# Kernel tuning notes

Hardware: AMD Instinct MI355X
Metric: run time of the kernel (lower is better)

Reference implementation:

```python
import jax, jax.numpy as jnp
import numpy as np

B, T, IDIM, ODIM, HDIM, CDIM = 8, 8192, 256, 256, 1024, 128


def setup_inputs() -> dict:
    key = jax.random.key(0)
    ks = jax.random.split(key, 7)
    s_enc = 1.0 / np.sqrt(IDIM)
    s_dec = 1.0 / np.sqrt(HDIM)
    return {
        "x": jax.random.normal(ks[0], (B, T, IDIM), jnp.float32),
        "mask_prev": jnp.zeros((B, T, HDIM), jnp.float32),
        "W_enc": jax.random.uniform(ks[1], (IDIM, HDIM), jnp.float32, -s_enc, s_enc),
        "b_enc": jax.random.uniform(ks[2], (HDIM,), jnp.float32, -s_enc, s_enc),
        "W_dec_self": jax.random.uniform(ks[3], (HDIM, IDIM), jnp.float32, -s_dec, s_dec),
        "b_dec_self": jax.random.uniform(ks[4], (IDIM,), jnp.float32, -s_dec, s_dec),
        "W_dec_src": jax.random.uniform(ks[5], (HDIM, ODIM), jnp.float32, -s_dec, s_dec),
        "b_dec_src": jax.random.uniform(ks[6], (ODIM,), jnp.float32, -s_dec, s_dec),
        "decoder_type": 0,  # 0 = 'self', 1 = 'src'
    }


def _topk_masks(h, cdim):
    # energy_pooling_mask with share=True: topk(k=2*cdim) of h^2 along hdim.
    energy = h * h  # [B,T,H]
    _, idx = jax.lax.top_k(energy, 2 * cdim)  # [B,T,2C] indices into H
    bi = jnp.arange(h.shape[0])[:, None, None]
    ti = jnp.arange(h.shape[1])[None, :, None]
    # scatter instead of materializing one_hot [B,T,2C,H]
    mask = jnp.zeros_like(h).at[bi, ti, idx[..., :cdim]].add(1.0)
    mask_share = jnp.zeros_like(h).at[bi, ti, idx].add(1.0)
    return mask, mask_share


def reference(x, mask_prev, W_enc, b_enc, W_dec_self, b_dec_self, W_dec_src, b_dec_src, decoder_type):
    # encoder
    h = jnp.einsum("bti,ih->bth", x, W_enc) + b_enc  # [B,T,H]
    # hidden_exclude_activation (mask_prev provided): zero previously-used units
    h = jnp.where(mask_prev > 0, 0.0, h)
    mask_cur, mask_cur_share = _topk_masks(h, CDIM)
    mask_new = mask_prev + mask_cur
    h = jnp.where(mask_cur_share > 0, h, 0.0)
    # decoder (idim == odim asserted in original)
    if decoder_type == 0:
        out = jnp.einsum("bth,ho->bto", h, W_dec_self) + b_dec_self
    else:
        out = jnp.einsum("bth,ho->bto", h, W_dec_src) + b_dec_src
    return out, mask_new
```

## Files before the change

### kernel.cpp

```cpp
#include <hip/hip_runtime.h>
#include <hip/hip_bf16.h>

#define B_ 8
#define T_ 8192
#define M_ (B_ * T_)
#define IDIM 256
#define HDIM 1024
#define ODIM 256
#define CDIM 128
#define OUT_OFF ((size_t)M_ * ODIM)

typedef __attribute__((ext_vector_type(4))) float floatx4;
typedef __attribute__((ext_vector_type(8))) short shortx8;

__device__ __forceinline__ void glds16(const float* g, void* lds) {
    __builtin_amdgcn_global_load_lds(
        (const __attribute__((address_space(1))) void*)g,
        (__attribute__((address_space(3))) void*)lds, 16, 0, 0);
}

__global__ __launch_bounds__(256) void k0_convw(const float* __restrict__ Wself,
                                                const float* __restrict__ Wsrc,
                                                const int* __restrict__ dtype,
                                                __hip_bfloat16* __restrict__ WdT) {
    int id = blockIdx.x * 256 + threadIdx.x;
    int n = id >> 10;
    int k = id & 1023;
    const float* W = (*dtype == 0) ? Wself : Wsrc;
    WdT[id] = __float2bfloat16(W[(size_t)k * ODIM + n]);
}

__global__ __launch_bounds__(256, 3) void k1_enc(const float* __restrict__ X,
                                                 const float* __restrict__ W,
                                                 const float* __restrict__ bias,
                                                 float* __restrict__ H) {
    __shared__ __align__(16) float As[32][128];
    __shared__ __align__(16) float Bs[2][32][128];
    const int t  = threadIdx.x;
    const int m0 = blockIdx.x * 128;
    const int n0 = blockIdx.y * 128;
    const int tx = t & 15;
    const int ty = t >> 4;
    const int wavebase = t & ~63;

    int acol[4], ak4[4];
    const float* aptr[4];
#pragma unroll
    for (int r = 0; r < 4; ++r) {
        int idx = r * 256 + t;
        int row = idx >> 3;
        int k4  = (idx & 7) << 2;
        ak4[r]  = k4;
        acol[r] = row ^ k4;
        aptr[r] = X + (size_t)(m0 + row) * IDIM + k4;
    }
    const float* bptr[4];
#pragma unroll
    for (int r = 0; r < 4; ++r) {
        int idx = r * 256 + t;
        int row = idx >> 5;
        int c4  = (idx & 31) << 2;
        bptr[r] = W + (size_t)row * HDIM + n0 + c4;
    }

    float acc[8][8];
#pragma unroll
    for (int i = 0; i < 8; ++i)
#pragma unroll
        for (int j = 0; j < 8; ++j) acc[i][j] = 0.0f;

    float4 areg[4];

#pragma unroll
    for (int r = 0; r < 4; ++r) areg[r] = *(const float4*)(aptr[r]);
#pragma unroll
    for (int r = 0; r < 4; ++r)
        glds16(bptr[r], (char*)&Bs[0][0][0] + (size_t)(r * 256 + wavebase) * 16);
#pragma unroll
    for (int r = 0; r < 4; ++r) {
        As[ak4[r] + 0][acol[r]] = areg[r].x;
        As[ak4[r] + 1][acol[r]] = areg[r].y;
        As[ak4[r] + 2][acol[r]] = areg[r].z;
        As[ak4[r] + 3][acol[r]] = areg[r].w;
    }
    asm volatile("s_waitcnt vmcnt(0)");
    __syncthreads();

#pragma unroll 1
    for (int tt = 0; tt < IDIM / 32; ++tt) {
        const int cur = tt & 1;
        if (tt < IDIM / 32 - 1) {
            const int kn = (tt + 1) * 32;
#pragma unroll
            for (int r = 0; r < 4; ++r)
                glds16(bptr[r] + (size_t)kn * HDIM,
                       (char*)&Bs[cur ^ 1][0][0] + (size_t)(r * 256 + wavebase) * 16);
#pragma unroll
            for (int r = 0; r < 4; ++r) areg[r] = *(const float4*)(aptr[r] + kn);
        }

#pragma unroll 8
        for (int k = 0; k < 32; ++k) {
            const int s = k & 28;
            float4 a0 = *(const float4*)&As[k][(ty * 8) ^ s];
            float4 a1 = *(const float4*)&As[k][(ty * 8 + 4) ^ s];
            float4 b0 = *(const float4*)&Bs[cur][k][tx * 4];
            float4 b1 = *(const float4*)&Bs[cur][k][tx * 4 + 64];
#define FMA_ROW(i, ax)                              \
            acc[i][0] = fmaf(ax, b0.x, acc[i][0]);  \
            acc[i][1] = fmaf(ax, b0.y, acc[i][1]);  \
            acc[i][2] = fmaf(ax, b0.z, acc[i][2]);  \
            acc[i][3] = fmaf(ax, b0.w, acc[i][3]);  \
            acc[i][4] = fmaf(ax, b1.x, acc[i][4]);  \
            acc[i][5] = fmaf(ax, b1.y, acc[i][5]);  \
            acc[i][6] = fmaf(ax, b1.z, acc[i][6]);  \
            acc[i][7] = fmaf(ax, b1.w, acc[i][7]);
            FMA_ROW(0, a0.x) FMA_ROW(1, a0.y) FMA_ROW(2, a0.z) FMA_ROW(3, a0.w)
            FMA_ROW(4, a1.x) FMA_ROW(5, a1.y) FMA_ROW(6, a1.z) FMA_ROW(7, a1.w)
#undef FMA_ROW
        }

        if (tt < IDIM / 32 - 1) {
            asm volatile("s_waitcnt vmcnt(0)");
            __syncthreads();
#pragma unroll
            for (int r = 0; r < 4; ++r) {
                As[ak4[r] + 0][acol[r]] = areg[r].x;
                As[ak4[r] + 1][acol[r]] = areg[r].y;
                As[ak4[r] + 2][acol[r]] = areg[r].z;
                As[ak4[r] + 3][acol[r]] = areg[r].w;
            }
            __syncthreads();
        }
    }

#pragma unroll
    for (int i = 0; i < 8; ++i) {
        int gm = m0 + ty * 8 + i;
        float* o = H + (size_t)gm * HDIM + n0;
        float4 v0, v1;
        v0.x = acc[i][0] + bias[n0 + tx * 4 + 0];
        v0.y = acc[i][1] + bias[n0 + tx * 4 + 1];
        v0.z = acc[i][2] + bias[n0 + tx * 4 + 2];
        v0.w = acc[i][3] + bias[n0 + tx * 4 + 3];
        v1.x = acc[i][4] + bias[n0 + 64 + tx * 4 + 0];
        v1.y = acc[i][5] + bias[n0 + 64 + tx * 4 + 1];
        v1.z = acc[i][6] + bias[n0 + 64 + tx * 4 + 2];
        v1.w = acc[i][7] + bias[n0 + 64 + tx * 4 + 3];
        *(float4*)(o + tx * 4) = v0;
        *(float4*)(o + 64 + tx * 4) = v1;
    }
}

#define NBIN 512
#define KBASE 1600
#define CAP 128

__device__ __forceinline__ unsigned int bsearch_kth(const unsigned int* u, int k,
                                                    int lane, int* r_out) {
    unsigned long long lo = 0, hi = 0xFFFFFFFFull;
    while (lo < hi) {
        unsigned int mid = (unsigned int)((lo + hi + 1) >> 1);
        int c = 0;
#pragma unroll
        for (int i = 0; i < 16; ++i) c += (u[i] >= mid) ? 1 : 0;
#pragma unroll
        for (int off = 1; off < 64; off <<= 1) {
            int o = __shfl_down(c, off, 64);
            if (lane + off < 64) c += o;
        }
        c = __shfl(c, 0);
        if (c >= k) lo = mid; else hi = (unsigned long long)mid - 1;
    }
    unsigned int T = (unsigned int)lo;
    int g = 0;
#pragma unroll
    for (int i = 0; i < 16; ++i) g += (u[i] > T) ? 1 : 0;
#pragma unroll
    for (int off = 1; off < 64; off <<= 1) {
        int o = __shfl_down(g, off, 64);
        if (lane + off < 64) g += o;
    }
    g = __shfl(g, 0);
    *r_out = k - g;
    return T;
}

__global__ __launch_bounds__(64) void k2_topk(const float* __restrict__ mask_prev,
                                              float* __restrict__ Hio,
                                              __hip_bfloat16* __restrict__ Abf) {
    __shared__ unsigned int hist[NBIN];
    __shared__ unsigned long long cand[2][CAP];
    __shared__ unsigned int sres[8];
    __shared__ unsigned int scnt[2];
    const int lane = threadIdx.x;
    const size_t row = (size_t)blockIdx.x;
    const float* mp = mask_prev + row * HDIM + lane * 16;
    float* hrow = Hio + row * HDIM + lane * 16;

    float hv[16], mpv[16];
    unsigned int u[16];
    int bin[16];
#pragma unroll
    for (int c = 0; c < 4; ++c) {
        float4 m4 = *(const float4*)(mp + c * 4);
        float4 h4 = *(const float4*)(hrow + c * 4);
        float mm[4] = {m4.x, m4.y, m4.z, m4.w};
        float hh[4] = {h4.x, h4.y, h4.z, h4.w};
#pragma unroll
        for (int x = 0; x < 4; ++x) {
            int i = c * 4 + x;
            float h = (mm[x] > 0.0f) ? 0.0f : hh[x];
            mpv[i] = mm[x]; hv[i] = h;
            u[i] = __float_as_uint(h * h);
            int b = (int)(u[i] >> 19) - KBASE;
            bin[i] = (b < 0) ? 0 : ((b > NBIN - 1) ? NBIN - 1 : b);
        }
    }

#pragma unroll
    for (int q = 0; q < 8; ++q) hist[lane + (q << 6)] = 0u;
    if (lane < 2) scnt[lane] = 0u;
    __syncthreads();
#pragma unroll
    for (int i = 0; i < 16; ++i) atomicAdd(&hist[bin[i]], 1u);
    __syncthreads();

    {
        unsigned int cj[8]; unsigned int lt = 0;
#pragma unroll
        for (int jj = 0; jj < 8; ++jj) { cj[jj] = hist[lane * 8 + jj]; lt += cj[jj]; }
        unsigned int s = lt;
#pragma unroll
        for (int off = 1; off < 64; off <<= 1) {
            unsigned int o = (unsigned int)__shfl_down((int)s, off, 64);
            if (lane + off < 64) s += o;
        }
        unsigned int run = s - lt;
#pragma unroll
        for (int jj = 7; jj >= 0; --jj) {
            unsigned int gt = run, ge = run + cj[jj];
            if (gt < CDIM && CDIM <= ge)         { sres[0] = lane * 8 + jj; sres[1] = CDIM - gt; }
            if (gt < 2 * CDIM && 2 * CDIM <= ge) { sres[2] = lane * 8 + jj; sres[3] = 2 * CDIM - gt; }
            run = ge;
        }
    }
    __syncthreads();
    const unsigned int b1 = sres[0], kk1 = sres[1];
    const unsigned int b2 = sres[2], kk2 = sres[3];

#pragma unroll
    for (int i = 0; i < 16; ++i) {
        int j = lane * 16 + i;
        unsigned long long pk = ((unsigned long long)u[i] << 32) | (unsigned int)(1023 - j);
        if ((unsigned int)bin[i] == b1) {
            unsigned int p = atomicAdd(&scnt[0], 1u);
            if (p < CAP) cand[0][p] = pk;
        }
        if (b2 != b1 && (unsigned int)bin[i] == b2) {
            unsigned int p = atomicAdd(&scnt[1], 1u);
            if (p < CAP) cand[1][p] = pk;
        }
    }
    __syncthreads();
    const unsigned int C1 = scnt[0];
    const unsigned int C2 = (b2 == b1) ? C1 : scnt[1];
    const unsigned long long* L2 = (b2 == b1) ? cand[0] : cand[1];

    if (C1 <= CAP) {
        for (unsigned int idx = lane; idx < C1; idx += 64) {
            unsigned long long mine = cand[0][idx];
            unsigned int myu = (unsigned int)(mine >> 32);
            unsigned int rank = 0, gtu = 0;
            for (unsigned int c = 0; c < C1; ++c) {
                unsigned long long o = cand[0][c];
                rank += (o > mine) ? 1u : 0u;
                gtu  += ((unsigned int)(o >> 32) > myu) ? 1u : 0u;
            }
            if (rank == kk1 - 1) { sres[4] = myu; sres[5] = gtu; }
        }
    }
    if (C2 <= CAP) {
        for (unsigned int idx = lane; idx < C2; idx += 64) {
            unsigned long long mine = L2[idx];
            unsigned int myu = (unsigned int)(mine >> 32);
            unsigned int rank = 0, gtu = 0;
            for (unsigned int c = 0; c < C2; ++c) {
                unsigned long long o = L2[c];
                rank += (o > mine) ? 1u : 0u;
                gtu  += ((unsigned int)(o >> 32) > myu) ? 1u : 0u;
            }
            if (rank == kk2 - 1) { sres[6] = myu; sres[7] = gtu; }
        }
    }
    __syncthreads();

    unsigned int T1, T2; int r1, r2;
    if (C1 <= CAP) { T1 = sres[4]; r1 = (int)(kk1 - sres[5]); }
    else           { T1 = bsearch_kth(u, CDIM, lane, &r1); }
    if (C2 <= CAP) { T2 = sres[6]; r2 = (int)(kk2 - sres[7]); }
    else           { T2 = bsearch_kth(u, 2 * CDIM, lane, &r2); }

    int p1[16], p2[16];
    int tot1 = 0, tot2 = 0;
#pragma unroll
    for (int i = 0; i < 16; ++i) {
        p1[i] = tot1; p2[i] = tot2;
        tot1 += (u[i] == T1) ? 1 : 0;
        tot2 += (u[i] == T2) ? 1 : 0;
    }
    int s1v = tot1, s2v = tot2;
#pragma unroll
    for (int off = 1; off < 64; off <<= 1) {
        int o1 = __shfl_up(s1v, off, 64);
        int o2 = __shfl_up(s2v, off, 64);
        if (lane >= off) { s1v += o1; s2v += o2; }
    }
    const int ex1 = s1v - tot1;
    const int ex2 = s2v - tot2;

#pragma unroll
    for (int c = 0; c < 4; ++c) {
        float v[4];
#pragma unroll
        for (int x = 0; x < 4; ++x) {
            int i = c * 4 + x;
            bool s1 = (u[i] > T1) || ((u[i] == T1) && (ex1 + p1[i] < r1));
            v[x] = mpv[i] + (s1 ? 1.0f : 0.0f);
        }
        float4 v4 = {v[0], v[1], v[2], v[3]};
        *(float4*)(hrow + c * 4) = v4;
    }
    __hip_bfloat16* ab = Abf + row * HDIM + lane * 16;
#pragma unroll
    for (int half = 0; half < 2; ++half) {
        union { unsigned short us[8]; uint4 v; } pk;
#pragma unroll
        for (int x = 0; x < 8; ++x) {
            int i = half * 8 + x;
            bool s2 = (u[i] > T2) || ((u[i] == T2) && (ex2 + p2[i] < r2));
            __hip_bfloat16 bb = __float2bfloat16(s2 ? hv[i] : 0.0f);
            pk.us[x] = *(unsigned short*)&bb;
        }
        *(uint4*)(ab + half * 8) = pk.v;
    }
}

#define K3LD 40
__global__ __launch_bounds__(256) void k3_dec(const __hip_bfloat16* __restrict__ A,
                                              const __hip_bfloat16* __restrict__ Bt,
                                              const float* __restrict__ bias_self,
                                              const float* __restrict__ bias_src,
                                              const int* __restrict__ dtype,
                                              float* __restrict__ Out) {
    __shared__ __align__(16) __hip_bfloat16 As[128 * K3LD];
    __shared__ __align__(16) __hip_bfloat16 Bs[128 * K3LD];
    const int t = threadIdx.x;
    const int lane = t & 63;
    const int wave = t >> 6;
    const int m0 = blockIdx.x * 128;
    const int n0 = blockIdx.y * 128;
    const int wr = wave >> 1;
    const int wc = wave & 1;
    const int quad = lane >> 4;
    const int rf = lane & 15;

    int srow[2], skc[2];
#pragma unroll
    for (int p = 0; p < 2; ++p) {
        int l = p * 256 + t;
        srow[p] = l >> 2;
        skc[p]  = (l & 3) << 3;
    }

    floatx4 acc[4][4];
    const floatx4 z = {0.0f, 0.0f, 0.0f, 0.0f};
#pragma unroll
    for (int i = 0; i < 4; ++i)
#pragma unroll
        for (int j = 0; j < 4; ++j) acc[i][j] = z;

    uint4 apre[2], bpre[2];
#pragma unroll
    for (int p = 0; p < 2; ++p) {
        apre[p] = *(const uint4*)(A  + (size_t)(m0 + srow[p]) * HDIM + skc[p]);
        bpre[p] = *(const uint4*)(Bt + (size_t)(n0 + srow[p]) * HDIM + skc[p]);
    }
#pragma unroll
    for (int p = 0; p < 2; ++p) {
        *(uint4*)&As[srow[p] * K3LD + skc[p]] = apre[p];
        *(uint4*)&Bs[srow[p] * K3LD + skc[p]] = bpre[p];
    }
    __syncthreads();

#pragma unroll 1
    for (int kt = 0; kt < HDIM / 32; ++kt) {
        if (kt < HDIM / 32 - 1) {
            int kn = (kt + 1) * 32;
#pragma unroll
            for (int p = 0; p < 2; ++p) {
                apre[p] = *(const uint4*)(A  + (size_t)(m0 + srow[p]) * HDIM + kn + skc[p]);
                bpre[p] = *(const uint4*)(Bt + (size_t)(n0 + srow[p]) * HDIM + kn + skc[p]);
            }
        }
        shortx8 af[4], bf[4];
#pragma unroll
        for (int i = 0; i < 4; ++i) {
            af[i] = *(const shortx8*)&As[(wr * 64 + i * 16 + rf) * K3LD + quad * 8];
            bf[i] = *(const shortx8*)&Bs[(wc * 64 + i * 16 + rf) * K3LD + quad * 8];
        }
#pragma unroll
        for (int mi = 0; mi < 4; ++mi)
#pragma unroll
            for (int nj = 0; nj < 4; ++nj)
                acc[mi][nj] = __builtin_amdgcn_mfma_f32_16x16x32_bf16(
                    af[mi], bf[nj], acc[mi][nj], 0, 0, 0);
        __syncthreads();
        if (kt < HDIM / 32 - 1) {
#pragma unroll
            for (int p = 0; p < 2; ++p) {
                *(uint4*)&As[srow[p] * K3LD + skc[p]] = apre[p];
                *(uint4*)&Bs[srow[p] * K3LD + skc[p]] = bpre[p];
            }
            __syncthreads();
        }
    }

    const float* bias = (*dtype == 0) ? bias_self : bias_src;
#pragma unroll
    for (int mi = 0; mi < 4; ++mi) {
#pragma unroll
        for (int nj = 0; nj < 4; ++nj) {
            int gn = n0 + wc * 64 + nj * 16 + rf;
            float bv = bias[gn];
            int gmb = m0 + wr * 64 + mi * 16 + quad * 4;
#pragma unroll
            for (int r2 = 0; r2 < 4; ++r2)
                Out[(size_t)(gmb + r2) * ODIM + gn] = acc[mi][nj][r2] + bv;
        }
    }
}

extern "C" void kernel_launch(void* const* d_in, const int* in_sizes, int n_in,
                              void* d_out, int out_size, void* d_ws, size_t ws_size,
                              hipStream_t stream) {
    const float* x          = (const float*)d_in[0];
    const float* mask_prev  = (const float*)d_in[1];
    const float* W_enc      = (const float*)d_in[2];
    const float* b_enc      = (const float*)d_in[3];
    const float* W_dec_self = (const float*)d_in[4];
    const float* b_dec_self = (const float*)d_in[5];
    const float* W_dec_src  = (const float*)d_in[6];
    const float* b_dec_src  = (const float*)d_in[7];
    const int*   dtype      = (const int*)d_in[8];

    float* out  = (float*)d_out;
    float* Hbuf = out + OUT_OFF;

    __hip_bfloat16* Abf = (__hip_bfloat16*)d_ws;
    __hip_bfloat16* WdT = (__hip_bfloat16*)((char*)d_ws + (size_t)M_ * HDIM * 2);

    k0_convw<<<dim3((ODIM * HDIM) / 256), 256, 0, stream>>>(W_dec_self, W_dec_src, dtype, WdT);
    k1_enc  <<<dim3(M_ / 128, HDIM / 128), 256, 0, stream>>>(x, W_enc, b_enc, Hbuf);
    k2_topk <<<dim3(M_), 64, 0, stream>>>(mask_prev, Hbuf, Abf);
    k3_dec  <<<dim3(M_ / 128, ODIM / 128), 256, 0, stream>>>(Abf, WdT, b_dec_self, b_dec_src, dtype, out);
}
```

Baseline: 1.175 ms.

## Double-buffer decoder GEMM tiles with direct global-to-LDS loads

The decoder GEMM now stages A and B tiles straight from global memory into LDS with global_load_lds into two buffers, so the next k-tile loads while the current one feeds the MFMAs. This drops the register staging, the explicit LDS stores and one barrier per iteration, and sets launch bounds to two blocks per CU. The LDS row stride loses its padding (32 instead of 40), so fragment reads may hit more bank conflicts. The decoder is a small share of total time.

```diff
diff --git a/kernel.cpp b/kernel.cpp
--- a/kernel.cpp
+++ b/kernel.cpp
@@ -13,7 +13,7 @@
 typedef __attribute__((ext_vector_type(4))) float floatx4;
 typedef __attribute__((ext_vector_type(8))) short shortx8;
 
-__device__ __forceinline__ void glds16(const float* g, void* lds) {
+__device__ __forceinline__ void glds16(const void* g, void* lds) {
     __builtin_amdgcn_global_load_lds(
         (const __attribute__((address_space(1))) void*)g,
         (__attribute__((address_space(3))) void*)lds, 16, 0, 0);
@@ -346,15 +346,14 @@
     }
 }
 
-#define K3LD 40
-__global__ __launch_bounds__(256) void k3_dec(const __hip_bfloat16* __restrict__ A,
-                                              const __hip_bfloat16* __restrict__ Bt,
-                                              const float* __restrict__ bias_self,
-                                              const float* __restrict__ bias_src,
-                                              const int* __restrict__ dtype,
-                                              float* __restrict__ Out) {
-    __shared__ __align__(16) __hip_bfloat16 As[128 * K3LD];
-    __shared__ __align__(16) __hip_bfloat16 Bs[128 * K3LD];
+__global__ __launch_bounds__(256, 2) void k3_dec(const __hip_bfloat16* __restrict__ A,
+                                                 const __hip_bfloat16* __restrict__ Bt,
+                                                 const float* __restrict__ bias_self,
+                                                 const float* __restrict__ bias_src,
+                                                 const int* __restrict__ dtype,
+                                                 float* __restrict__ Out) {
+    __shared__ __align__(16) __hip_bfloat16 As[2][128][32];
+    __shared__ __align__(16) __hip_bfloat16 Bs[2][128][32];
     const int t = threadIdx.x;
     const int lane = t & 63;
     const int wave = t >> 6;
@@ -364,13 +363,17 @@
     const int wc = wave & 1;
     const int quad = lane >> 4;
     const int rf = lane & 15;
-
-    int srow[2], skc[2];
+    const int wavebase = t & ~63;
+
+    const __hip_bfloat16* aptr[2];
+    const __hip_bfloat16* bptr[2];
 #pragma unroll
     for (int p = 0; p < 2; ++p) {
-        int l = p * 256 + t;
-        srow[p] = l >> 2;
-        skc[p]  = (l & 3) << 3;
+        int idx = p * 256 + t;
+        int row = idx >> 2;
+        int kc8 = (idx & 3) << 3;
+        aptr[p] = A  + (size_t)(m0 + row) * HDIM + kc8;
+        bptr[p] = Bt + (size_t)(n0 + row) * HDIM + kc8;
     }
 
     floatx4 acc[4][4];
@@ -380,34 +383,33 @@
 #pragma unroll
         for (int j = 0; j < 4; ++j) acc[i][j] = z;
 
-    uint4 apre[2], bpre[2];
 #pragma unroll
     for (int p = 0; p < 2; ++p) {
-        apre[p] = *(const uint4*)(A  + (size_t)(m0 + srow[p]) * HDIM + skc[p]);
-        bpre[p] = *(const uint4*)(Bt + (size_t)(n0 + srow[p]) * HDIM + skc[p]);
-    }
-#pragma unroll
-    for (int p = 0; p < 2; ++p) {
-        *(uint4*)&As[srow[p] * K3LD + skc[p]] = apre[p];
-        *(uint4*)&Bs[srow[p] * K3LD + skc[p]] = bpre[p];
-    }
+        glds16(aptr[p], (char*)&As[0][0][0] + (size_t)(p * 256 + wavebase) * 16);
+        glds16(bptr[p], (char*)&Bs[0][0][0] + (size_t)(p * 256 + wavebase) * 16);
+    }
+    asm volatile("s_waitcnt vmcnt(0)");
     __syncthreads();
 
 #pragma unroll 1
     for (int kt = 0; kt < HDIM / 32; ++kt) {
+        const int cur = kt & 1;
         if (kt < HDIM / 32 - 1) {
-            int kn = (kt + 1) * 32;
+            const int kn = (kt + 1) * 32;
 #pragma unroll
             for (int p = 0; p < 2; ++p) {
-                apre[p] = *(const uint4*)(A  + (size_t)(m0 + srow[p]) * HDIM + kn + skc[p]);
-                bpre[p] = *(const uint4*)(Bt + (size_t)(n0 + srow[p]) * HDIM + kn + skc[p]);
+                glds16(aptr[p] + kn,
+                       (char*)&As[cur ^ 1][0][0] + (size_t)(p * 256 + wavebase) * 16);
+                glds16(bptr[p] + kn,
+                       (char*)&Bs[cur ^ 1][0][0] + (size_t)(p * 256 + wavebase) * 16);
             }
         }
+
         shortx8 af[4], bf[4];
 #pragma unroll
         for (int i = 0; i < 4; ++i) {
-            af[i] = *(const shortx8*)&As[(wr * 64 + i * 16 + rf) * K3LD + quad * 8];
-            bf[i] = *(const shortx8*)&Bs[(wc * 64 + i * 16 + rf) * K3LD + quad * 8];
+            af[i] = *(const shortx8*)&As[cur][wr * 64 + i * 16 + rf][quad * 8];
+            bf[i] = *(const shortx8*)&Bs[cur][wc * 64 + i * 16 + rf][quad * 8];
         }
 #pragma unroll
         for (int mi = 0; mi < 4; ++mi)
@@ -415,13 +417,9 @@
             for (int nj = 0; nj < 4; ++nj)
                 acc[mi][nj] = __builtin_amdgcn_mfma_f32_16x16x32_bf16(
                     af[mi], bf[nj], acc[mi][nj], 0, 0, 0);
-        __syncthreads();
+
         if (kt < HDIM / 32 - 1) {
-#pragma unroll
-            for (int p = 0; p < 2; ++p) {
-                *(uint4*)&As[srow[p] * K3LD + skc[p]] = apre[p];
-                *(uint4*)&Bs[srow[p] * K3LD + skc[p]] = bpre[p];
-            }
+            asm volatile("s_waitcnt vmcnt(0)");
             __syncthreads();
         }
     }
```

New measurement: 1.055 ms. 1.11x faster.
